# Kernel optimization log

Measured on AMD Instinct MI355X. Metric: run time of the kernel, lower is better.

The kernel has to match this reference:

```python
import jax, jax.numpy as jnp
import numpy as np

DIM = 1024
NUM_HEADS = 16
HEAD_DIM = DIM // NUM_HEADS
SCALE = 1.0 / float(np.sqrt(HEAD_DIM))


def setup_inputs() -> dict:
    key = jax.random.key(0)
    ks = jax.random.split(key, 5)
    B, S = 2, 2048
    x = jax.random.normal(ks[0], (B, S, DIM), dtype=jnp.float32)
    qkv_w = jax.random.normal(ks[1], (3 * DIM, DIM), dtype=jnp.float32) * (1.0 / np.sqrt(DIM))
    qkv_b = jax.random.normal(ks[2], (3 * DIM,), dtype=jnp.float32) * 0.02
    proj_w = jax.random.normal(ks[3], (DIM, DIM), dtype=jnp.float32) * (1.0 / np.sqrt(DIM))
    proj_b = jax.random.normal(ks[4], (DIM,), dtype=jnp.float32) * 0.02
    return {"x": x, "qkv_w": qkv_w, "qkv_b": qkv_b, "proj_w": proj_w, "proj_b": proj_b}


def reference(x, qkv_w, qkv_b, proj_w, proj_b):
    B, S, _ = x.shape
    # qkv projection: (B,S,3*DIM) -> (3, B, H, S, Dh)
    qkv = x @ qkv_w.T + qkv_b
    qkv = qkv.reshape(B, S, 3, NUM_HEADS, HEAD_DIM).transpose(2, 0, 3, 1, 4)
    q, k, v = qkv[0], qkv[1], qkv[2]
    # scaled dot-product attention (full score matrix, as in the original)
    scores = jnp.einsum('bhqd,bhkd->bhqk', q, k) * SCALE
    attn = jax.nn.softmax(scores, axis=-1)
    out = jnp.einsum('bhqk,bhkd->bhqd', attn, v)  # (B,H,S,Dh)
    out = out.transpose(0, 2, 1, 3).reshape(B, S, DIM)
    return out @ proj_w.T + proj_b
```

## Files before the change

### kernel.cpp

```cpp
#include <hip/hip_runtime.h>

#define DIM_ 1024
#define NH_ 16
#define HD_ 64
#define B_ 2
#define S_ 2048
#define M_ (B_ * S_)
#define NQKV_ (3 * DIM_)

typedef __attribute__((ext_vector_type(8))) __bf16 bf16x8;
typedef __attribute__((ext_vector_type(4))) __bf16 bf16x4;
typedef __attribute__((ext_vector_type(4))) float f32x4;

__device__ __forceinline__ void gl_lds16(const void* g, void* l) {
  __builtin_amdgcn_global_load_lds(
      (__attribute__((address_space(1))) void*)const_cast<void*>(g),
      (__attribute__((address_space(3))) void*)l, 16, 0, 0);
}

#define N4_X 1048576
#define N4_W1 786432
#define N4_W2 262144
__global__ __launch_bounds__(256) void cast_all(const float* __restrict__ x,
                                                const float* __restrict__ w1,
                                                const float* __restrict__ w2,
                                                __bf16* __restrict__ xb,
                                                __bf16* __restrict__ w1b,
                                                __bf16* __restrict__ w2b) {
  int i = blockIdx.x * 256 + threadIdx.x;
  const int stride = gridDim.x * 256;
  for (; i < N4_X + N4_W1 + N4_W2; i += stride) {
    const float4* src;
    bf16x4* dst;
    int j;
    if (i < N4_X) { src = (const float4*)x; dst = (bf16x4*)xb; j = i; }
    else if (i < N4_X + N4_W1) { src = (const float4*)w1; dst = (bf16x4*)w1b; j = i - N4_X; }
    else { src = (const float4*)w2; dst = (bf16x4*)w2b; j = i - (N4_X + N4_W1); }
    float4 v = src[j];
    bf16x4 o;
    o[0] = (__bf16)v.x; o[1] = (__bf16)v.y; o[2] = (__bf16)v.z; o[3] = (__bf16)v.w;
    dst[j] = o;
  }
}

template <int MODE, int BM>
__global__ __launch_bounds__(512, 4) void gemm_bt(const __bf16* __restrict__ A,
                                                  const __bf16* __restrict__ Bw,
                                                  const float* __restrict__ bias,
                                                  __bf16* __restrict__ Qp, __bf16* __restrict__ Kp,
                                                  __bf16* __restrict__ Vt,
                                                  float* __restrict__ Cout) {
  constexpr int KD = 1024;
  constexpr int BN = 128;
  constexpr int MT = BM / 64;
  constexpr int NC = (BM + BN) / 64;
  __shared__ __bf16 As[BM * 64];
  __shared__ __bf16 Bs[BN * 64];
  const int tid = threadIdx.x;
  const int lane = tid & 63;
  const int wave = tid >> 6;
  const int quad = lane >> 4;
  const int r16 = lane & 15;
  const int wm = wave >> 1;
  const int wn = wave & 1;
  const int m0 = blockIdx.y * BM;
  const int n0 = blockIdx.x * BN;

  const f32x4 fz = {0.f, 0.f, 0.f, 0.f};
  f32x4 acc[MT][4];
#pragma unroll
  for (int i = 0; i < MT; ++i)
#pragma unroll
    for (int j = 0; j < 4; ++j) acc[i][j] = fz;

  const __bf16* gp[NC];
  __bf16* lp[NC];
#pragma unroll
  for (int i = 0; i < NC; ++i) {
    const int c = tid + i * 512;
    if (c < BM * 8) {
      const int r = c >> 3, cc = c & 7;
      gp[i] = A + (size_t)(m0 + r) * KD + ((cc ^ (r & 7)) * 8);
      lp[i] = &As[c * 8];
    } else {
      const int c2 = c - BM * 8;
      const int r = c2 >> 3, cc = c2 & 7;
      gp[i] = Bw + (size_t)(n0 + r) * KD + ((cc ^ (r & 7)) * 8);
      lp[i] = &Bs[c2 * 8];
    }
  }

  for (int kt = 0; kt < KD / 64; ++kt) {
    __syncthreads();
#pragma unroll
    for (int i = 0; i < NC; ++i) { gl_lds16(gp[i], lp[i]); gp[i] += 64; }
    __syncthreads();

#pragma unroll
    for (int sub = 0; sub < 2; ++sub) {
      const int ch = ((sub * 4 + quad) ^ (r16 & 7)) * 8;
      bf16x8 af[MT], bfr[4];
#pragma unroll
      for (int mt = 0; mt < MT; ++mt)
        af[mt] = *(const bf16x8*)&As[(wm * MT * 16 + mt * 16 + r16) * 64 + ch];
#pragma unroll
      for (int nt = 0; nt < 4; ++nt)
        bfr[nt] = *(const bf16x8*)&Bs[(wn * 64 + nt * 16 + r16) * 64 + ch];
#pragma unroll
      for (int mt = 0; mt < MT; ++mt)
#pragma unroll
        for (int nt = 0; nt < 4; ++nt)
          acc[mt][nt] =
              __builtin_amdgcn_mfma_f32_16x16x32_bf16(af[mt], bfr[nt], acc[mt][nt], 0, 0, 0);
    }
  }

  if (MODE == 0) {
#pragma unroll
    for (int nt = 0; nt < 4; ++nt) {
      const int n = n0 + wn * 64 + nt * 16 + r16;
      const int sel = n >> 10;
      const int h = (n >> 6) & 15;
      const int dh = n & 63;
      const float bs = bias[n];
      if (sel == 2) {
#pragma unroll
        for (int mt = 0; mt < MT; ++mt) {
          const int m = m0 + wm * MT * 16 + mt * 16 + quad * 4;
          const int b = m >> 11;
          const int s = m & 2047;
          const int slot = (s & ~31) | (((s >> 2) & 3) << 3) | (((s >> 4) & 1) << 2);
          bf16x4 ov;
#pragma unroll
          for (int r = 0; r < 4; ++r) ov[r] = (__bf16)(acc[mt][nt][r] + bs);
          *(bf16x4*)&Vt[((size_t)((b * NH_ + h) * HD_ + dh)) * S_ + slot] = ov;
        }
      } else {
        __bf16* dst = (sel == 0) ? Qp : Kp;
        const float mul = (sel == 0) ? 0.18033688011112042f : 1.0f;
#pragma unroll
        for (int mt = 0; mt < MT; ++mt) {
#pragma unroll
          for (int r = 0; r < 4; ++r) {
            const int m = m0 + wm * MT * 16 + mt * 16 + quad * 4 + r;
            const int b = m >> 11;
            const int s = m & 2047;
            dst[((size_t)((b * NH_ + h) * S_ + s)) * HD_ + dh] =
                (__bf16)((acc[mt][nt][r] + bs) * mul);
          }
        }
      }
    }
  } else {
#pragma unroll
    for (int nt = 0; nt < 4; ++nt) {
      const int n = n0 + wn * 64 + nt * 16 + r16;
      const float bs = bias[n];
#pragma unroll
      for (int mt = 0; mt < MT; ++mt) {
#pragma unroll
        for (int r = 0; r < 4; ++r) {
          const int m = m0 + wm * MT * 16 + mt * 16 + quad * 4 + r;
          Cout[(size_t)m * DIM_ + n] = acc[mt][nt][r] + bs;
        }
      }
    }
  }
}

__global__ __launch_bounds__(512) void attn(const __bf16* __restrict__ Qp,
                                            const __bf16* __restrict__ Kp,
                                            const __bf16* __restrict__ Vtp,
                                            __bf16* __restrict__ ctx) {
  __shared__ __bf16 Ks[2][128 * 64];
  __shared__ __bf16 Vs[2][64 * 128];
  const int tid = threadIdx.x;
  const int lane = tid & 63;
  const int wave = tid >> 6;
  const int quad = lane >> 4;
  const int r16 = lane & 15;
  const int bh = blockIdx.y;
  const int q0 = blockIdx.x * 128;
  const int qrow = q0 + wave * 16 + r16;

  const __bf16* qb = Qp + ((size_t)bh * S_ + qrow) * HD_;
  const bf16x8 qf0 = *(const bf16x8*)(qb + quad * 8);
  const bf16x8 qf1 = *(const bf16x8*)(qb + 32 + quad * 8);

  const f32x4 fz = {0.f, 0.f, 0.f, 0.f};
  f32x4 o[4];
#pragma unroll
  for (int d = 0; d < 4; ++d) o[d] = fz;
  float lsum = 0.f;

  const __bf16* gk[2];
  const __bf16* gv[2];
  int lofs[2];
#pragma unroll
  for (int i = 0; i < 2; ++i) {
    const int c = tid + i * 512;
    const int kr = c >> 3, kc = c & 7;
    gk[i] = Kp + ((size_t)bh * S_ + kr) * HD_ + ((kc ^ (kr & 7)) * 8);
    const int vr = c >> 4, vc = c & 15;
    gv[i] = Vtp + ((size_t)bh * HD_ + vr) * S_ + ((vc ^ (vr & 15)) * 8);
    lofs[i] = c * 8;
  }

#pragma unroll
  for (int i = 0; i < 2; ++i) {
    gl_lds16(gk[i], &Ks[0][lofs[i]]); gk[i] += 128 * HD_;
    gl_lds16(gv[i], &Vs[0][lofs[i]]); gv[i] += 128;
  }

  for (int kt = 0; kt < S_ / 128; ++kt) {
    const int cb = kt & 1;
    __syncthreads();
    if (kt + 1 < S_ / 128) {
#pragma unroll
      for (int i = 0; i < 2; ++i) {
        gl_lds16(gk[i], &Ks[cb ^ 1][lofs[i]]); gk[i] += 128 * HD_;
        gl_lds16(gv[i], &Vs[cb ^ 1][lofs[i]]); gv[i] += 128;
      }
    }

    f32x4 sa[8];
#pragma unroll
    for (int mt = 0; mt < 8; ++mt) {
      const int row = mt * 16 + r16;
      bf16x8 k0 = *(const bf16x8*)&Ks[cb][row * 64 + ((quad ^ (row & 7)) * 8)];
      bf16x8 k1 = *(const bf16x8*)&Ks[cb][row * 64 + (((4 + quad) ^ (row & 7)) * 8)];
      f32x4 t = fz;
      t = __builtin_amdgcn_mfma_f32_16x16x32_bf16(k0, qf0, t, 0, 0, 0);
      t = __builtin_amdgcn_mfma_f32_16x16x32_bf16(k1, qf1, t, 0, 0, 0);
      sa[mt] = t;
    }

    bf16x8 pf[4];
#pragma unroll
    for (int ks = 0; ks < 4; ++ks)
#pragma unroll
      for (int r = 0; r < 4; ++r) {
        float p0 = __builtin_amdgcn_exp2f(sa[2 * ks][r]);
        float p1 = __builtin_amdgcn_exp2f(sa[2 * ks + 1][r]);
        lsum += p0 + p1;
        pf[ks][r] = (__bf16)p0;
        pf[ks][4 + r] = (__bf16)p1;
      }

#pragma unroll
    for (int ks = 0; ks < 4; ++ks)
#pragma unroll
      for (int dt = 0; dt < 4; ++dt) {
        const int row = dt * 16 + r16;
        bf16x8 va = *(const bf16x8*)&Vs[cb][row * 128 + (((4 * ks + quad) ^ (row & 15)) * 8)];
        o[dt] = __builtin_amdgcn_mfma_f32_16x16x32_bf16(va, pf[ks], o[dt], 0, 0, 0);
      }
  }

  lsum += __shfl_xor(lsum, 16);
  lsum += __shfl_xor(lsum, 32);
  const float inv = 1.0f / lsum;
  const int b = bh >> 4, h = bh & 15;
  const int s = q0 + wave * 16 + r16;
#pragma unroll
  for (int dt = 0; dt < 4; ++dt) {
    bf16x4 ov;
#pragma unroll
    for (int r = 0; r < 4; ++r) ov[r] = (__bf16)(o[dt][r] * inv);
    *(bf16x4*)&ctx[((size_t)(b * S_ + s)) * DIM_ + h * 64 + dt * 16 + quad * 4] = ov;
  }
}

extern "C" void kernel_launch(void* const* d_in, const int* in_sizes, int n_in, void* d_out,
                              int out_size, void* d_ws, size_t ws_size, hipStream_t stream) {
  const float* x = (const float*)d_in[0];
  const float* qkv_w = (const float*)d_in[1];
  const float* qkv_b = (const float*)d_in[2];
  const float* proj_w = (const float*)d_in[3];
  const float* proj_b = (const float*)d_in[4];
  float* out = (float*)d_out;

  char* ws = (char*)d_ws;
  __bf16* Xb = (__bf16*)(ws);
  __bf16* Wb = (__bf16*)(ws + 8388608);
  __bf16* Pb = (__bf16*)(ws + 14680064);
  __bf16* Qp = (__bf16*)(ws + 16777216);
  __bf16* Kp = (__bf16*)(ws + 25165824);
  __bf16* Vt = (__bf16*)(ws + 33554432);
  __bf16* Cx = (__bf16*)(ws + 41943040);

  cast_all<<<2048, 256, 0, stream>>>(x, qkv_w, proj_w, Xb, Wb, Pb);
  gemm_bt<0, 128><<<dim3(NQKV_ / 128, M_ / 128), 512, 0, stream>>>(Xb, Wb, qkv_b, Qp, Kp, Vt,
                                                                   nullptr);
  attn<<<dim3(S_ / 128, 32), 512, 0, stream>>>(Qp, Kp, Vt, Cx);
  gemm_bt<1, 64><<<dim3(DIM_ / 128, M_ / 64), 512, 0, stream>>>(Cx, Pb, proj_b, nullptr, nullptr,
                                                                nullptr, out);
}
```

Before: 170.5 us.

## Give each attention wave two query tiles with 256-thread blocks and swizzled grid

The attention kernel now uses 256-thread blocks in which each wave handles 32 query rows as two 16-row tiles. Every K and V fragment read from LDS feeds two MFMAs, which halves LDS read traffic per unit of compute. The block-to-(head, query tile) mapping is remapped so consecutive blocks share heads, which should improve L2 reuse of K/V. The score and PV phases are interleaved per 32-key chunk to limit register pressure, though the doubled accumulators still raise VGPR use, and occupancy is hinted via launch_bounds(256,2).

```diff
diff --git a/kernel.cpp b/kernel.cpp
--- a/kernel.cpp
+++ b/kernel.cpp
@@ -168,10 +168,10 @@
   }
 }
 
-__global__ __launch_bounds__(512) void attn(const __bf16* __restrict__ Qp,
-                                            const __bf16* __restrict__ Kp,
-                                            const __bf16* __restrict__ Vtp,
-                                            __bf16* __restrict__ ctx) {
+__global__ __launch_bounds__(256, 2) void attn(const __bf16* __restrict__ Qp,
+                                               const __bf16* __restrict__ Kp,
+                                               const __bf16* __restrict__ Vtp,
+                                               __bf16* __restrict__ ctx) {
   __shared__ __bf16 Ks[2][128 * 64];
   __shared__ __bf16 Vs[2][64 * 128];
   const int tid = threadIdx.x;
@@ -179,26 +179,30 @@
   const int wave = tid >> 6;
   const int quad = lane >> 4;
   const int r16 = lane & 15;
-  const int bh = blockIdx.y;
-  const int q0 = blockIdx.x * 128;
-  const int qrow = q0 + wave * 16 + r16;
-
-  const __bf16* qb = Qp + ((size_t)bh * S_ + qrow) * HD_;
-  const bf16x8 qf0 = *(const bf16x8*)(qb + quad * 8);
-  const bf16x8 qf1 = *(const bf16x8*)(qb + 32 + quad * 8);
+
+  const int w = blockIdx.y * 16 + blockIdx.x;
+  const int bh = (w & 7) + (((w >> 3) >> 4) << 3);
+  const int q0 = ((w >> 3) & 15) * 128;
+
+  const __bf16* qg0 = Qp + ((size_t)bh * S_ + (q0 + wave * 32 + r16)) * HD_;
+  const __bf16* qg1 = qg0 + 16 * HD_;
+  const bf16x8 qa0 = *(const bf16x8*)(qg0 + quad * 8);
+  const bf16x8 qa1 = *(const bf16x8*)(qg0 + 32 + quad * 8);
+  const bf16x8 qc0 = *(const bf16x8*)(qg1 + quad * 8);
+  const bf16x8 qc1 = *(const bf16x8*)(qg1 + 32 + quad * 8);
 
   const f32x4 fz = {0.f, 0.f, 0.f, 0.f};
-  f32x4 o[4];
-#pragma unroll
-  for (int d = 0; d < 4; ++d) o[d] = fz;
-  float lsum = 0.f;
-
-  const __bf16* gk[2];
-  const __bf16* gv[2];
-  int lofs[2];
-#pragma unroll
-  for (int i = 0; i < 2; ++i) {
-    const int c = tid + i * 512;
+  f32x4 o0[4], o1[4];
+#pragma unroll
+  for (int d = 0; d < 4; ++d) { o0[d] = fz; o1[d] = fz; }
+  float ls0 = 0.f, ls1 = 0.f;
+
+  const __bf16* gk[4];
+  const __bf16* gv[4];
+  int lofs[4];
+#pragma unroll
+  for (int i = 0; i < 4; ++i) {
+    const int c = tid + i * 256;
     const int kr = c >> 3, kc = c & 7;
     gk[i] = Kp + ((size_t)bh * S_ + kr) * HD_ + ((kc ^ (kr & 7)) * 8);
     const int vr = c >> 4, vc = c & 15;
@@ -207,7 +211,7 @@
   }
 
 #pragma unroll
-  for (int i = 0; i < 2; ++i) {
+  for (int i = 0; i < 4; ++i) {
     gl_lds16(gk[i], &Ks[0][lofs[i]]); gk[i] += 128 * HD_;
     gl_lds16(gv[i], &Vs[0][lofs[i]]); gv[i] += 128;
   }
@@ -217,57 +221,74 @@
     __syncthreads();
     if (kt + 1 < S_ / 128) {
 #pragma unroll
-      for (int i = 0; i < 2; ++i) {
+      for (int i = 0; i < 4; ++i) {
         gl_lds16(gk[i], &Ks[cb ^ 1][lofs[i]]); gk[i] += 128 * HD_;
         gl_lds16(gv[i], &Vs[cb ^ 1][lofs[i]]); gv[i] += 128;
       }
     }
 
-    f32x4 sa[8];
-#pragma unroll
-    for (int mt = 0; mt < 8; ++mt) {
-      const int row = mt * 16 + r16;
-      bf16x8 k0 = *(const bf16x8*)&Ks[cb][row * 64 + ((quad ^ (row & 7)) * 8)];
-      bf16x8 k1 = *(const bf16x8*)&Ks[cb][row * 64 + (((4 + quad) ^ (row & 7)) * 8)];
-      f32x4 t = fz;
-      t = __builtin_amdgcn_mfma_f32_16x16x32_bf16(k0, qf0, t, 0, 0, 0);
-      t = __builtin_amdgcn_mfma_f32_16x16x32_bf16(k1, qf1, t, 0, 0, 0);
-      sa[mt] = t;
-    }
-
-    bf16x8 pf[4];
-#pragma unroll
-    for (int ks = 0; ks < 4; ++ks)
+#pragma unroll
+    for (int ks = 0; ks < 4; ++ks) {
+      const int row0 = ks * 32 + r16;
+      const int row1 = row0 + 16;
+      const int xa = (quad ^ (r16 & 7)) * 8;
+      const int xb = ((4 + quad) ^ (r16 & 7)) * 8;
+      const bf16x8 k00 = *(const bf16x8*)&Ks[cb][row0 * 64 + xa];
+      const bf16x8 k01 = *(const bf16x8*)&Ks[cb][row0 * 64 + xb];
+      const bf16x8 k10 = *(const bf16x8*)&Ks[cb][row1 * 64 + xa];
+      const bf16x8 k11 = *(const bf16x8*)&Ks[cb][row1 * 64 + xb];
+      f32x4 t00 = fz, t01 = fz, t10 = fz, t11 = fz;
+      t00 = __builtin_amdgcn_mfma_f32_16x16x32_bf16(k00, qa0, t00, 0, 0, 0);
+      t00 = __builtin_amdgcn_mfma_f32_16x16x32_bf16(k01, qa1, t00, 0, 0, 0);
+      t01 = __builtin_amdgcn_mfma_f32_16x16x32_bf16(k10, qa0, t01, 0, 0, 0);
+      t01 = __builtin_amdgcn_mfma_f32_16x16x32_bf16(k11, qa1, t01, 0, 0, 0);
+      t10 = __builtin_amdgcn_mfma_f32_16x16x32_bf16(k00, qc0, t10, 0, 0, 0);
+      t10 = __builtin_amdgcn_mfma_f32_16x16x32_bf16(k01, qc1, t10, 0, 0, 0);
+      t11 = __builtin_amdgcn_mfma_f32_16x16x32_bf16(k10, qc0, t11, 0, 0, 0);
+      t11 = __builtin_amdgcn_mfma_f32_16x16x32_bf16(k11, qc1, t11, 0, 0, 0);
+
+      bf16x8 pf0, pf1;
 #pragma unroll
       for (int r = 0; r < 4; ++r) {
-        float p0 = __builtin_amdgcn_exp2f(sa[2 * ks][r]);
-        float p1 = __builtin_amdgcn_exp2f(sa[2 * ks + 1][r]);
-        lsum += p0 + p1;
-        pf[ks][r] = (__bf16)p0;
-        pf[ks][4 + r] = (__bf16)p1;
-      }
-
-#pragma unroll
-    for (int ks = 0; ks < 4; ++ks)
+        const float p00 = __builtin_amdgcn_exp2f(t00[r]);
+        const float p01 = __builtin_amdgcn_exp2f(t01[r]);
+        const float p10 = __builtin_amdgcn_exp2f(t10[r]);
+        const float p11 = __builtin_amdgcn_exp2f(t11[r]);
+        ls0 += p00 + p01;
+        ls1 += p10 + p11;
+        pf0[r] = (__bf16)p00; pf0[4 + r] = (__bf16)p01;
+        pf1[r] = (__bf16)p10; pf1[4 + r] = (__bf16)p11;
+      }
+
 #pragma unroll
       for (int dt = 0; dt < 4; ++dt) {
         const int row = dt * 16 + r16;
-        bf16x8 va = *(const bf16x8*)&Vs[cb][row * 128 + (((4 * ks + quad) ^ (row & 15)) * 8)];
-        o[dt] = __builtin_amdgcn_mfma_f32_16x16x32_bf16(va, pf[ks], o[dt], 0, 0, 0);
-      }
-  }
-
-  lsum += __shfl_xor(lsum, 16);
-  lsum += __shfl_xor(lsum, 32);
-  const float inv = 1.0f / lsum;
+        const bf16x8 va = *(const bf16x8*)&Vs[cb][row * 128 + (((4 * ks + quad) ^ r16) * 8)];
+        o0[dt] = __builtin_amdgcn_mfma_f32_16x16x32_bf16(va, pf0, o0[dt], 0, 0, 0);
+        o1[dt] = __builtin_amdgcn_mfma_f32_16x16x32_bf16(va, pf1, o1[dt], 0, 0, 0);
+      }
+    }
+  }
+
+  ls0 += __shfl_xor(ls0, 16);
+  ls0 += __shfl_xor(ls0, 32);
+  ls1 += __shfl_xor(ls1, 16);
+  ls1 += __shfl_xor(ls1, 32);
+  const float inv0 = 1.0f / ls0;
+  const float inv1 = 1.0f / ls1;
   const int b = bh >> 4, h = bh & 15;
-  const int s = q0 + wave * 16 + r16;
+  const int s0 = q0 + wave * 32 + r16;
+  const int s1 = s0 + 16;
 #pragma unroll
   for (int dt = 0; dt < 4; ++dt) {
-    bf16x4 ov;
-#pragma unroll
-    for (int r = 0; r < 4; ++r) ov[r] = (__bf16)(o[dt][r] * inv);
-    *(bf16x4*)&ctx[((size_t)(b * S_ + s)) * DIM_ + h * 64 + dt * 16 + quad * 4] = ov;
+    bf16x4 ov0, ov1;
+#pragma unroll
+    for (int r = 0; r < 4; ++r) {
+      ov0[r] = (__bf16)(o0[dt][r] * inv0);
+      ov1[r] = (__bf16)(o1[dt][r] * inv1);
+    }
+    *(bf16x4*)&ctx[((size_t)(b * S_ + s0)) * DIM_ + h * 64 + dt * 16 + quad * 4] = ov0;
+    *(bf16x4*)&ctx[((size_t)(b * S_ + s1)) * DIM_ + h * 64 + dt * 16 + quad * 4] = ov1;
   }
 }
 
@@ -292,7 +313,7 @@
   cast_all<<<2048, 256, 0, stream>>>(x, qkv_w, proj_w, Xb, Wb, Pb);
   gemm_bt<0, 128><<<dim3(NQKV_ / 128, M_ / 128), 512, 0, stream>>>(Xb, Wb, qkv_b, Qp, Kp, Vt,
                                                                    nullptr);
-  attn<<<dim3(S_ / 128, 32), 512, 0, stream>>>(Qp, Kp, Vt, Cx);
+  attn<<<dim3(S_ / 128, 32), 256, 0, stream>>>(Qp, Kp, Vt, Cx);
   gemm_bt<1, 64><<<dim3(DIM_ / 128, M_ / 64), 512, 0, stream>>>(Cx, Pb, proj_b, nullptr, nullptr,
                                                                 nullptr, out);
 }
```

New measurement: 166.8 us. -2.2%, faster.
